# Optimization experiments

Measured on AMD Instinct MI355X. Metric: run time of the kernel, lower is better.

## Reference

```python
import jax, jax.numpy as jnp
import numpy as np

DIM = 1024
HEADS = 8
DIM_HEAD = 64
INNER = HEADS * DIM_HEAD  # 512
N_PATCHES = 256
SCALE = DIM_HEAD ** -0.5


def setup_inputs() -> dict:
    key = jax.random.key(0)
    ks = jax.random.split(key, 6)
    s = lambda fan_in: 1.0 / np.sqrt(fan_in)
    return {
        "x": jax.random.normal(ks[0], (64, N_PATCHES, DIM), dtype=jnp.float32),
        "Wq": jax.random.normal(ks[1], (DIM, INNER), dtype=jnp.float32) * s(DIM),
        "Wkv": jax.random.normal(ks[2], (DIM, 2 * INNER), dtype=jnp.float32) * s(DIM),
        "Wout": jax.random.normal(ks[3], (INNER, DIM), dtype=jnp.float32) * s(INNER),
        "bout": jax.random.normal(ks[4], (DIM,), dtype=jnp.float32) * 0.01,
        "Wspec": jax.random.normal(ks[5], (N_PATCHES, 3 * N_PATCHES), dtype=jnp.float32) * s(N_PATCHES),
    }


def reference(x, Wq, Wkv, Wout, bout, Wspec):
    b, n, d = x.shape
    # ---- spatial: single center-query attention ----
    x_center = x[:, n // 2, :]                      # [b, d]
    q = (x_center @ Wq).reshape(b, HEADS, DIM_HEAD)  # [b, h, dh]
    kv = x @ Wkv                                     # [b, n, 2*inner]
    k, v = jnp.split(kv, 2, axis=-1)
    k = k.reshape(b, n, HEADS, DIM_HEAD).transpose(0, 2, 1, 3)  # [b, h, n, dh]
    v = v.reshape(b, n, HEADS, DIM_HEAD).transpose(0, 2, 1, 3)
    logits = jnp.einsum('bhd,bhnd->bhn', q, k) * SCALE
    attn = jax.nn.softmax(logits, axis=-1)           # [b, h, n]
    out = jnp.einsum('bhn,bhnd->bhd', attn, v).reshape(b, INNER)
    # torch expands attn over n identical rows BEFORE to_out; the rows are
    # identical, so broadcasting the projected row is the same math.
    spatial = out @ Wout + bout                      # [b, d]
    spatial_out = jnp.broadcast_to(spatial[:, None, :], (b, n, d))
    # ---- spectral: attention over transposed (feature) axis ----
    x_t = x.transpose(0, 2, 1)                       # [b, d, n]
    qkv = x_t @ Wspec                                # [b, d, 3n]
    q_s, k_s, v_s = jnp.split(qkv, 3, axis=-1)       # v_s unused (as in source)
    spec_logits = jnp.einsum('bin,bjn->bij', q_s, k_s) * SCALE  # [b, d, d]
    spec_weights = jax.nn.softmax(spec_logits, axis=-1)
    return jnp.einsum('bnd,bde->bne', spatial_out, spec_weights)
```

## Files before the change

kernel.cpp:

```cpp
#include <hip/hip_runtime.h>
#include <hip/hip_bf16.h>
#include <cstdint>

typedef _Float16 f16;
typedef _Float16 half8 __attribute__((ext_vector_type(8)));
typedef float f32x4 __attribute__((ext_vector_type(4)));

#define SCALE 0.125f

#define GLL(src, dst) __builtin_amdgcn_global_load_lds( \
    (const __attribute__((address_space(1))) unsigned int*)(src), \
    (__attribute__((address_space(3))) unsigned int*)(dst), 16, 0, 0)

__global__ __launch_bounds__(256) void prep_xT(const float* __restrict__ x, f16* __restrict__ xT) {
  __shared__ f16 tile[32][33];
  int b = blockIdx.z, nt = blockIdx.y, dt = blockIdx.x;
  int c = threadIdx.x & 31, rp = threadIdx.x >> 5;
  const float* xb = x + ((size_t)b*256 + nt*32)*1024 + dt*32;
#pragma unroll
  for (int p = 0; p < 4; ++p) { int r = p*8 + rp; tile[r][c] = (f16)xb[(size_t)r*1024 + c]; }
  __syncthreads();
  f16* o = xT + ((size_t)b*1024 + dt*32)*256 + nt*32;
#pragma unroll
  for (int p = 0; p < 4; ++p) { int r = p*8 + rp; o[(size_t)r*256 + c] = tile[c][r]; }
}

__global__ __launch_bounds__(256) void prep_Wspec16(const float* __restrict__ W, f16* __restrict__ Wt) {
  int row = blockIdx.x, t = threadIdx.x;
  Wt[(size_t)row*512 + t]       = (f16)W[(size_t)row*768 + t];
  Wt[(size_t)row*512 + 256 + t] = (f16)W[(size_t)row*768 + 256 + t];
}

template<int KSTEPS, int AST, int BST, int CST, bool SCALEQ>
__global__ __launch_bounds__(256) void gemm128(const f16* __restrict__ Ag, const f16* __restrict__ Bg,
                                               f16* __restrict__ Cg, size_t aB, size_t bB, size_t cB) {
  __shared__ f16 As[2][128*32];
  __shared__ f16 Bs[2][128*32];
  const f16* A = Ag + (size_t)blockIdx.z*aB;
  const f16* B = Bg + (size_t)blockIdx.z*bB;
  f16* C = Cg + (size_t)blockIdx.z*cB;
  int t = threadIdx.x, lane = t & 63, wave = t >> 6;
  int l15 = lane & 15, l4 = lane >> 4;
  int wm = wave & 1, wn = wave >> 1;
  size_t m0 = (size_t)blockIdx.x*128, n0 = (size_t)blockIdx.y*128;
  f32x4 acc[4][4];
#pragma unroll
  for (int i=0;i<4;++i)
#pragma unroll
    for (int j=0;j<4;++j) acc[i][j] = (f32x4){0.f,0.f,0.f,0.f};
  int rowS[2], chS[2];
#pragma unroll
  for (int c=0;c<2;++c) {
    int slot = c*256 + t;
    rowS[c] = slot >> 2;
    chS[c]  = (slot & 3) ^ ((slot >> 3) & 3);
  }
  int pc = (l4 ^ ((l15 >> 1) & 3)) * 8;

  auto STAGE = [&](int buf, int ks) {
    int k0 = ks*32;
#pragma unroll
    for (int c=0;c<2;++c) {
      GLL(A + (m0 + rowS[c])*(size_t)AST + k0 + chS[c]*8, &As[buf][(c*256 + wave*64)*8]);
      GLL(B + (n0 + rowS[c])*(size_t)BST + k0 + chS[c]*8, &Bs[buf][(c*256 + wave*64)*8]);
    }
  };

  STAGE(0, 0);
#pragma unroll 2
  for (int ks = 0; ks < KSTEPS; ++ks) {
    int cur = ks & 1;
    if (ks + 1 < KSTEPS) {
      STAGE(cur ^ 1, ks + 1);
      asm volatile("s_waitcnt vmcnt(4)" ::: "memory");
    } else {
      asm volatile("s_waitcnt vmcnt(0)" ::: "memory");
    }
    __builtin_amdgcn_s_barrier();
    __builtin_amdgcn_sched_barrier(0);
    half8 a[4], bb[4];
    const f16* Af = &As[cur][(wm*64 + l15)*32 + pc];
    const f16* Bf = &Bs[cur][(wn*64 + l15)*32 + pc];
#pragma unroll
    for (int mi=0;mi<4;++mi) a[mi]  = *(const half8*)(Af + mi*16*32);
#pragma unroll
    for (int ni=0;ni<4;++ni) bb[ni] = *(const half8*)(Bf + ni*16*32);
    __builtin_amdgcn_s_setprio(1);
#pragma unroll
    for (int mi=0;mi<4;++mi)
#pragma unroll
      for (int ni=0;ni<4;++ni)
        acc[mi][ni] = __builtin_amdgcn_mfma_f32_16x16x32_f16(a[mi], bb[ni], acc[mi][ni], 0,0,0);
    __builtin_amdgcn_s_setprio(0);
    __builtin_amdgcn_sched_barrier(0);
    __builtin_amdgcn_s_barrier();
  }
  float cscale = SCALEQ ? SCALE : 1.0f;
#pragma unroll
  for (int mi=0;mi<4;++mi)
#pragma unroll
    for (int ni=0;ni<4;++ni)
#pragma unroll
      for (int j=0;j<4;++j) {
        size_t row = m0 + wm*64 + mi*16 + 4*l4 + j;
        size_t col = n0 + wn*64 + ni*16 + l15;
        C[row*CST + col] = (f16)(acc[mi][ni][j] * cscale);
      }
}

__global__ __launch_bounds__(256) void qk(const float* __restrict__ x, const float* __restrict__ Wq,
                                          float* __restrict__ qbuf) {
  int b = blockIdx.x, h = blockIdx.y;
  int t = threadIdx.x;
  __shared__ float xc[1024];
  __shared__ float part[4][64];
  const float* xcg = x + ((size_t)b*256 + 128)*1024;
#pragma unroll
  for (int i = 0; i < 4; ++i) xc[t + 256*i] = xcg[t + 256*i];
  __syncthreads();
  int d = t & 63, chunk = t >> 6;
  float s = 0.f;
  const float* wq = Wq + (size_t)(chunk*256)*512 + h*64 + d;
#pragma unroll 8
  for (int c = 0; c < 256; ++c) s += xc[chunk*256 + c] * wq[(size_t)c*512];
  part[chunk][d] = s;
  __syncthreads();
  if (t < 64) qbuf[(size_t)b*512 + h*64 + t] = part[0][t]+part[1][t]+part[2][t]+part[3][t];
}

__global__ __launch_bounds__(256) void uk(const float* __restrict__ Wkv, const float* __restrict__ qbuf,
                                          f16* __restrict__ u16) {
  int h = blockIdx.x, dc = blockIdx.y;
  int t = threadIdx.x;
  __shared__ float Wk[32][64];
  __shared__ float qT[64][65];
  {
    int j = t & 63, g = t >> 6;
#pragma unroll
    for (int rr = 0; rr < 8; ++rr) {
      int dd = g*8 + rr;
      Wk[dd][j] = Wkv[(size_t)(dc*32 + dd)*1024 + h*64 + j];
    }
#pragma unroll
    for (int rr = 0; rr < 16; ++rr) {
      int bb = g*16 + rr;
      qT[j][bb] = qbuf[(size_t)bb*512 + h*64 + j];
    }
  }
  __syncthreads();
  int b = t & 63, dq = t >> 6;
#pragma unroll
  for (int i = 0; i < 8; ++i) {
    int dd = dq*8 + i;
    float s = 0.f;
#pragma unroll 8
    for (int j = 0; j < 64; ++j) s += qT[j][b] * Wk[dd][j];
    u16[((size_t)b*16 + h)*1024 + dc*32 + dd]       = (f16)s;
    u16[((size_t)b*16 + 8 + h)*1024 + dc*32 + dd]   = (f16)0.f;
  }
}

__global__ __launch_bounds__(64) void lgk(const float* __restrict__ x, const f16* __restrict__ u16,
                                          float* __restrict__ logitbuf) {
  int mt = blockIdx.x, b = blockIdx.y;
  int lane = threadIdx.x, l15 = lane & 15, l4 = lane >> 4;
  const float* Ap = x + ((size_t)b*256 + mt*16 + l15)*1024 + 8*l4;
  const f16* Bp = u16 + ((size_t)b*16 + l15)*1024 + 8*l4;
  f32x4 acc = (f32x4){0.f,0.f,0.f,0.f};
#pragma unroll 8
  for (int ks = 0; ks < 32; ++ks) {
    f32x4 lo = *(const f32x4*)(Ap + ks*32);
    f32x4 hi = *(const f32x4*)(Ap + ks*32 + 4);
    half8 h;
    h[0]=(f16)lo[0]; h[1]=(f16)lo[1]; h[2]=(f16)lo[2]; h[3]=(f16)lo[3];
    h[4]=(f16)hi[0]; h[5]=(f16)hi[1]; h[6]=(f16)hi[2]; h[7]=(f16)hi[3];
    acc = __builtin_amdgcn_mfma_f32_16x16x32_f16(h, *(const half8*)(Bp + ks*32), acc, 0,0,0);
  }
  if (l15 < 8) {
#pragma unroll
    for (int j = 0; j < 4; ++j)
      logitbuf[((size_t)b*256 + mt*16 + 4*l4 + j)*8 + l15] = acc[j];
  }
}

__global__ __launch_bounds__(256) void sm(const float* __restrict__ logitbuf, f16* __restrict__ attnW) {
  int b = blockIdx.x, t = threadIdx.x;
  __shared__ float eL[256][9];
  __shared__ float Zs[8];
  float e[8];
  const float* lp = logitbuf + (size_t)b*256*8 + (size_t)t*8;
#pragma unroll
  for (int h = 0; h < 8; ++h) { e[h] = __expf(lp[h] * SCALE); eL[t][h] = e[h]; }
  __syncthreads();
  {
    int h = t >> 5, i = t & 31;
    float s = 0.f;
#pragma unroll
    for (int k = 0; k < 8; ++k) s += eL[i + 32*k][h];
#pragma unroll
    for (int o = 1; o < 32; o <<= 1) s += __shfl_xor(s, o);
    if (i == 0) Zs[h] = s;
  }
  __syncthreads();
#pragma unroll
  for (int h = 0; h < 8; ++h) attnW[((size_t)b*16 + h)*256 + t] = (f16)(e[h] / Zs[h]);
#pragma unroll
  for (int h = 8; h < 16; ++h) attnW[((size_t)b*16 + h)*256 + t] = (f16)0.f;
}

__global__ __launch_bounds__(64) void xbk(const f16* __restrict__ attnW, const f16* __restrict__ xT,
                                          f16* __restrict__ xbar) {
  int dt = blockIdx.x, b = blockIdx.y;
  int lane = threadIdx.x, l15 = lane & 15, l4 = lane >> 4;
  const f16* Ap = attnW + ((size_t)b*16 + l15)*256 + 8*l4;
  const f16* Bp = xT + ((size_t)b*1024 + dt*16 + l15)*256 + 8*l4;
  f32x4 acc = (f32x4){0.f,0.f,0.f,0.f};
#pragma unroll
  for (int ks = 0; ks < 8; ++ks)
    acc = __builtin_amdgcn_mfma_f32_16x16x32_f16(*(const half8*)(Ap + ks*32),
                                                 *(const half8*)(Bp + ks*32), acc, 0,0,0);
  if (l4 < 2) {
#pragma unroll
    for (int j = 0; j < 4; ++j)
      xbar[((size_t)b*8 + 4*l4 + j)*1024 + dt*16 + l15] = (f16)acc[j];
  }
}

__global__ __launch_bounds__(256) void vk(const f16* __restrict__ xbar, const float* __restrict__ Wkv,
                                          float* __restrict__ attnout) {
  int h = blockIdx.x, dc = blockIdx.y, bc = blockIdx.z;
  int t = threadIdx.x;
  __shared__ float Wv[256][64];
  {
    int j = t & 63, g = t >> 6;
#pragma unroll
    for (int rr = 0; rr < 64; ++rr) {
      int dd = g*64 + rr;
      Wv[dd][j] = Wkv[(size_t)(dc*256 + dd)*1024 + 512 + h*64 + j];
    }
  }
  __syncthreads();
  int j = t & 63, bq = t >> 6;
  float s[4] = {0.f,0.f,0.f,0.f};
  const f16* xp[4];
#pragma unroll
  for (int bl = 0; bl < 4; ++bl)
    xp[bl] = xbar + ((size_t)(bc*16 + bq*4 + bl)*8 + h)*1024 + dc*256;
  for (int d8 = 0; d8 < 32; ++d8) {
    half8 xv[4];
#pragma unroll
    for (int bl = 0; bl < 4; ++bl) xv[bl] = *(const half8*)(xp[bl] + d8*8);
#pragma unroll
    for (int i = 0; i < 8; ++i) {
      float w = Wv[d8*8 + i][j];
#pragma unroll
      for (int bl = 0; bl < 4; ++bl) s[bl] += (float)xv[bl][i] * w;
    }
  }
#pragma unroll
  for (int bl = 0; bl < 4; ++bl)
    atomicAdd(&attnout[(size_t)(bc*16 + bq*4 + bl)*512 + h*64 + j], s[bl]);
}

__global__ __launch_bounds__(256) void spatialf(const float* __restrict__ attnout, const float* __restrict__ Wout,
                                                const float* __restrict__ bout, float* __restrict__ spatial) {
  int ec = blockIdx.x, b = blockIdx.y;
  int t = threadIdx.x;
  __shared__ float ao[512];
  ao[t]       = attnout[(size_t)b*512 + t];
  ao[t + 256] = attnout[(size_t)b*512 + 256 + t];
  __syncthreads();
  int e = ec*256 + t;
  float a0 = bout[e], a1 = 0.f;
#pragma unroll 8
  for (int i = 0; i < 512; i += 2) {
    a0 += ao[i]     * Wout[(size_t)i*1024 + e];
    a1 += ao[i + 1] * Wout[(size_t)(i + 1)*1024 + e];
  }
  spatial[(size_t)b*1024 + e] = a0 + a1;
}

__global__ __launch_bounds__(1024, 4) void speck(const f16* __restrict__ Y, const f16* __restrict__ xT,
                                                 const float* __restrict__ spatial, float* __restrict__ r) {
  __shared__ __attribute__((aligned(16))) char smem[163840];
  f16* As = (f16*)smem;
  f16* Bs = (f16*)(smem + 32768);
  float* sz   = (float*)smem;
  float* zfin = (float*)(smem + 4096);
  int bid = blockIdx.x;
  int xcd = bid & 7, q = bid >> 3;
  int b = xcd*8 + (q >> 4);
  int iblk = q & 15;
  int t = threadIdx.x, lane = t & 63, wave = t >> 6;
  int l15 = lane & 15, l4 = lane >> 4;
  const f16* Yb  = Y  + (size_t)b*262144;
  const f16* xTb = xT + (size_t)b*262144;
  int i0 = iblk*64;

  f32x4 acc[4][4];
#pragma unroll
  for (int mi=0;mi<4;++mi)
#pragma unroll
    for (int ni=0;ni<4;++ni) acc[mi][ni] = (f32x4){0.f,0.f,0.f,0.f};
  int pc = (l4 ^ ((l15 >> 1) & 3)) * 8;

#pragma unroll
  for (int g = 0; g < 2; ++g) {
    int u = (wave*2 + g)*64 + lane;
    int rA = u >> 5, v = u & 31;
    int s = v ^ (rA & 7);
    GLL(Yb + (size_t)(i0 + rA)*256 + (s >> 2)*32 + (s & 3)*8, As + ((wave*2 + g)*64)*8);
  }
  auto STAGE_B = [&](int slot, int ks) {
    int k0 = ks*32;
#pragma unroll
    for (int c = 0; c < 4; ++c) {
      int u2 = c*64 + lane;
      int row = u2 >> 2, pchk = u2 & 3;
      int ch = pchk ^ (((row & 15) >> 1) & 3);
      GLL(xTb + (size_t)(wave*64 + row)*256 + k0 + ch*8,
          Bs + ((wave*2 + slot)*256 + c*64)*8);
    }
  };
  STAGE_B(0, 0);
  STAGE_B(1, 1);
  asm volatile("s_waitcnt vmcnt(8)" ::: "memory");
  __builtin_amdgcn_s_barrier();

  int axor = l15 & 7;
#pragma unroll
  for (int ks = 0; ks < 8; ++ks) {
    int slot = ks & 1;
    if (ks < 7) asm volatile("s_waitcnt vmcnt(4)" ::: "memory");
    else        asm volatile("s_waitcnt vmcnt(0)" ::: "memory");
    __builtin_amdgcn_sched_barrier(0);
    half8 a[4], bb[4];
    const f16* Bbase = Bs + (wave*2 + slot)*2048;
    int physA = ((ks*4 + l4) ^ axor)*8;
#pragma unroll
    for (int mi = 0; mi < 4; ++mi) a[mi]  = *(const half8*)(As + (mi*16 + l15)*256 + physA);
#pragma unroll
    for (int ni = 0; ni < 4; ++ni) bb[ni] = *(const half8*)(Bbase + (ni*16 + l15)*32 + pc);
    asm volatile("s_waitcnt lgkmcnt(0)" ::: "memory");
    __builtin_amdgcn_sched_barrier(0);
    if (ks < 6) STAGE_B(slot, ks + 2);
    __builtin_amdgcn_s_setprio(1);
#pragma unroll
    for (int ni = 0; ni < 4; ++ni)
#pragma unroll
      for (int mi = 0; mi < 4; ++mi)
        acc[mi][ni] = __builtin_amdgcn_mfma_f32_16x16x32_f16(a[mi], bb[ni], acc[mi][ni], 0,0,0);
    __builtin_amdgcn_s_setprio(0);
    __builtin_amdgcn_sched_barrier(0);
  }
  float zr[4][4];
#pragma unroll
  for (int mi=0;mi<4;++mi)
#pragma unroll
    for (int jj=0;jj<4;++jj) {
      float s = 0.f;
#pragma unroll
      for (int ni=0;ni<4;++ni) {
        float e = __expf(acc[mi][ni][jj]);
        acc[mi][ni][jj] = e;
        s += e;
      }
#pragma unroll
      for (int o=1;o<16;o<<=1) s += __shfl_xor(s, o);
      zr[mi][jj] = s;
    }
  __syncthreads();
  if (l15 == 0) {
#pragma unroll
    for (int mi=0;mi<4;++mi)
#pragma unroll
      for (int jj=0;jj<4;++jj) sz[(mi*16 + 4*l4 + jj)*16 + wave] = zr[mi][jj];
  }
  __syncthreads();
  {
    float v = sz[t];
#pragma unroll
    for (int o=1;o<16;o<<=1) v += __shfl_xor(v, o);
    if ((t & 15) == 0) zfin[t >> 4] = v;
  }
  __syncthreads();
  float f[4][4];
#pragma unroll
  for (int mi=0;mi<4;++mi)
#pragma unroll
    for (int jj=0;jj<4;++jj) {
      int row = mi*16 + 4*l4 + jj;
      f[mi][jj] = spatial[(size_t)b*1024 + i0 + row] / zfin[row];
    }
  float* rb = r + (size_t)b*1024;
#pragma unroll
  for (int ni=0;ni<4;++ni) {
    float v = 0.f;
#pragma unroll
    for (int mi=0;mi<4;++mi)
#pragma unroll
      for (int jj=0;jj<4;++jj) v += f[mi][jj]*acc[mi][ni][jj];
    v += __shfl_xor(v, 16);
    v += __shfl_xor(v, 32);
    if (l4 == 0) atomicAdd(rb + wave*64 + ni*16 + l15, v);
  }
}

__global__ __launch_bounds__(256) void bcast(const float* __restrict__ r, float* __restrict__ out) {
  size_t row = blockIdx.x;
  int b = (int)(row >> 8);
  f32x4 v = *(const f32x4*)(r + (size_t)b*1024 + threadIdx.x*4);
  *(f32x4*)(out + row*1024 + (size_t)threadIdx.x*4) = v;
}

extern "C" void kernel_launch(void* const* d_in, const int* in_sizes, int n_in,
                              void* d_out, int out_size, void* d_ws, size_t ws_size,
                              hipStream_t stream) {
  const float* x     = (const float*)d_in[0];
  const float* Wq    = (const float*)d_in[1];
  const float* Wkv   = (const float*)d_in[2];
  const float* Wout  = (const float*)d_in[3];
  const float* bout  = (const float*)d_in[4];
  const float* Wspec = (const float*)d_in[5];
  float* out = (float*)d_out;
  char* ws = (char*)d_ws;
  f16*   Ybuf     = (f16*)(ws);
  f16*   u16pad   = (f16*)(ws);
  float* logitbuf = (float*)(ws + 2097152);
  f16*   attnW    = (f16*)(ws + 2621440);
  f16*   xbar     = (f16*)(ws + 3145728);
  float* qbuf     = (float*)(ws + 5242880);
  f16*   MT       = (f16*)(ws + 33554432);
  f16*   xT       = (f16*)(ws + 67108864);
  f16*   Wspec16  = (f16*)(ws + 102760448);
  float* attnout  = (float*)(ws + 103022592);
  float* spatial  = (float*)(ws + 103153664);
  float* rvec     = (float*)(ws + 103415808);
  (void)in_sizes; (void)n_in; (void)out_size; (void)ws_size;

  prep_xT     <<<dim3(32, 8, 64), dim3(256), 0, stream>>>(x, xT);
  prep_Wspec16<<<dim3(256),       dim3(256), 0, stream>>>(Wspec, Wspec16);
  gemm128<8,512,512,256,false><<<dim3(2, 2, 1), dim3(256), 0, stream>>>(Wspec16 + 256, Wspec16, MT, 0, 0, 0);
  hipMemsetAsync(attnout, 0, 64*512*sizeof(float), stream);
  qk          <<<dim3(64, 8),     dim3(256), 0, stream>>>(x, Wq, qbuf);
  uk          <<<dim3(8, 32),     dim3(256), 0, stream>>>(Wkv, qbuf, u16pad);
  lgk         <<<dim3(16, 64),    dim3(64),  0, stream>>>(x, u16pad, logitbuf);
  sm          <<<dim3(64),        dim3(256), 0, stream>>>(logitbuf, attnW);
  xbk         <<<dim3(64, 64),    dim3(64),  0, stream>>>(attnW, xT, xbar);
  vk          <<<dim3(8, 4, 4),   dim3(256), 0, stream>>>(xbar, Wkv, attnout);
  spatialf    <<<dim3(4, 64),     dim3(256), 0, stream>>>(attnout, Wout, bout, spatial);
  gemm128<8,256,256,256,true><<<dim3(8, 2, 64), dim3(256), 0, stream>>>(xT, MT, Ybuf,
                                                                        262144, 0, 262144);
  hipMemsetAsync(rvec, 0, 64*1024*sizeof(float), stream);
  speck       <<<dim3(1024),      dim3(1024), 0, stream>>>(Ybuf, xT, spatial, rvec);
  bcast       <<<dim3(16384),     dim3(256), 0, stream>>>(rvec, out);
}
```

Measured before the change: 215.2 us.

## Fuse Y = xT·MT GEMM into spectral kernel prologue

Removes the separate gemm128 launch that produced the scaled Y buffer. The speck kernel now loads its 64-row slice of xT into shared memory, multiplies it by MT with MFMA (MT read directly from global memory), and writes the scaled f16 result back into the swizzled A tile before the main loop. This saves one launch and the global write and re-read of Y. In exchange, each block does extra MFMA work with unstaged global reads of MT and adds two block barriers.

```diff
diff --git a/kernel.cpp b/kernel.cpp
--- a/kernel.cpp
+++ b/kernel.cpp
@@ -280,7 +280,7 @@
   spatial[(size_t)b*1024 + e] = a0 + a1;
 }
 
-__global__ __launch_bounds__(1024, 4) void speck(const f16* __restrict__ Y, const f16* __restrict__ xT,
+__global__ __launch_bounds__(1024, 4) void speck(const f16* __restrict__ MT, const f16* __restrict__ xT,
                                                  const float* __restrict__ spatial, float* __restrict__ r) {
   __shared__ __attribute__((aligned(16))) char smem[163840];
   f16* As = (f16*)smem;
@@ -293,23 +293,15 @@
   int iblk = q & 15;
   int t = threadIdx.x, lane = t & 63, wave = t >> 6;
   int l15 = lane & 15, l4 = lane >> 4;
-  const f16* Yb  = Y  + (size_t)b*262144;
   const f16* xTb = xT + (size_t)b*262144;
   int i0 = iblk*64;
-
-  f32x4 acc[4][4];
-#pragma unroll
-  for (int mi=0;mi<4;++mi)
-#pragma unroll
-    for (int ni=0;ni<4;++ni) acc[mi][ni] = (f32x4){0.f,0.f,0.f,0.f};
-  int pc = (l4 ^ ((l15 >> 1) & 3)) * 8;
 
 #pragma unroll
   for (int g = 0; g < 2; ++g) {
     int u = (wave*2 + g)*64 + lane;
     int rA = u >> 5, v = u & 31;
     int s = v ^ (rA & 7);
-    GLL(Yb + (size_t)(i0 + rA)*256 + (s >> 2)*32 + (s & 3)*8, As + ((wave*2 + g)*64)*8);
+    GLL(xTb + (size_t)(i0 + rA)*256 + (s >> 2)*32 + (s & 3)*8, As + ((wave*2 + g)*64)*8);
   }
   auto STAGE_B = [&](int slot, int ks) {
     int k0 = ks*32;
@@ -327,7 +319,41 @@
   asm volatile("s_waitcnt vmcnt(8)" ::: "memory");
   __builtin_amdgcn_s_barrier();
 
+  int r0 = (wave & 3)*16, c0 = (wave >> 2)*64;
+  f32x4 accy[4];
+#pragma unroll
+  for (int ci = 0; ci < 4; ++ci) accy[ci] = (f32x4){0.f,0.f,0.f,0.f};
   int axor = l15 & 7;
+#pragma unroll
+  for (int ks = 0; ks < 8; ++ks) {
+    int physA = ((ks*4 + l4) ^ axor)*8;
+    half8 ax = *(const half8*)(As + (r0 + l15)*256 + physA);
+#pragma unroll
+    for (int ci = 0; ci < 4; ++ci) {
+      half8 bmt = *(const half8*)(MT + (size_t)(c0 + ci*16 + l15)*256 + ks*32 + 8*l4);
+      accy[ci] = __builtin_amdgcn_mfma_f32_16x16x32_f16(ax, bmt, accy[ci], 0,0,0);
+    }
+  }
+  __syncthreads();
+#pragma unroll
+  for (int ci = 0; ci < 4; ++ci) {
+    int col = c0 + ci*16 + l15;
+    int ls = col >> 3, off = col & 7;
+#pragma unroll
+    for (int jj = 0; jj < 4; ++jj) {
+      int row = r0 + 4*l4 + jj;
+      As[row*256 + ((ls ^ (row & 7))*8) + off] = (f16)(accy[ci][jj] * SCALE);
+    }
+  }
+  __syncthreads();
+
+  f32x4 acc[4][4];
+#pragma unroll
+  for (int mi=0;mi<4;++mi)
+#pragma unroll
+    for (int ni=0;ni<4;++ni) acc[mi][ni] = (f32x4){0.f,0.f,0.f,0.f};
+  int pc = (l4 ^ ((l15 >> 1) & 3)) * 8;
+
 #pragma unroll
   for (int ks = 0; ks < 8; ++ks) {
     int slot = ks & 1;
@@ -424,7 +450,6 @@
   const float* Wspec = (const float*)d_in[5];
   float* out = (float*)d_out;
   char* ws = (char*)d_ws;
-  f16*   Ybuf     = (f16*)(ws);
   f16*   u16pad   = (f16*)(ws);
   float* logitbuf = (float*)(ws + 2097152);
   f16*   attnW    = (f16*)(ws + 2621440);
@@ -449,9 +474,7 @@
   xbk         <<<dim3(64, 64),    dim3(64),  0, stream>>>(attnW, xT, xbar);
   vk          <<<dim3(8, 4, 4),   dim3(256), 0, stream>>>(xbar, Wkv, attnout);
   spatialf    <<<dim3(4, 64),     dim3(256), 0, stream>>>(attnout, Wout, bout, spatial);
-  gemm128<8,256,256,256,true><<<dim3(8, 2, 64), dim3(256), 0, stream>>>(xT, MT, Ybuf,
-                                                                        262144, 0, 262144);
   hipMemsetAsync(rvec, 0, 64*1024*sizeof(float), stream);
-  speck       <<<dim3(1024),      dim3(1024), 0, stream>>>(Ybuf, xT, spatial, rvec);
+  speck       <<<dim3(1024),      dim3(1024), 0, stream>>>(MT, xT, spatial, rvec);
   bcast       <<<dim3(16384),     dim3(256), 0, stream>>>(rvec, out);
 }
```

New measurement: 252.4 us. +17.3%, slower.
